# Optimization experiments

Measured on AMD Instinct MI355X. Metric: run time of the kernel, lower is better.

Reference implementation:

```python
import jax, jax.numpy as jnp
import numpy as np

B, C, T = 32, 1024, 1024
BETA = 0.95      # snn.Leaky(beta=0.95)
THR = 1.0        # snntorch Leaky default threshold
SIGMA_INIT = 10.5  # mean of sigma_range (1, 20)


def _gaussian_matrix(sigma, channels):
    # row i is the Gaussian pdf over x=0..C-1 centered at mean=i (vectorized
    # form of the source's per-row Python loop; identical values).
    x = jnp.arange(channels, dtype=jnp.float32)
    u = (x[None, :] - x[:, None]) / sigma  # [C, C]
    coef = 1.0 / (sigma * jnp.sqrt(jnp.asarray(2.0 * jnp.pi, dtype=jnp.float32)))
    return coef * jnp.exp(-0.5 * u * u)


def _spike(u):
    # heaviside(u) forward; ATan surrogate gradient (snntorch default, alpha=2)
    soft = jnp.arctan(jnp.pi * u) / jnp.pi
    hard = (u > 0).astype(u.dtype)
    return soft + jax.lax.stop_gradient(hard - soft)


def setup_inputs() -> dict:
    key = jax.random.key(0)
    inp = jax.random.normal(key, (B, C, T), dtype=jnp.float32)
    sigma = jnp.ones((1,), dtype=jnp.float32) * SIGMA_INIT
    return {"inp": inp, "sigma": sigma}


def reference(inp, sigma):
    # inp: [B, C, T], sigma: [1]
    s = sigma[0]
    w = _gaussian_matrix(s, inp.shape[1])  # computed once: identical at every t
    # I[b,i,t] = x[b,i,t] - sum_j w[i,j] * x[b,j,t]
    I = inp - jnp.einsum('ij,bjt->bit', w, inp)
    I_tbc = jnp.moveaxis(I, 2, 0)  # [T, B, C]

    def step(mem, It):
        # snntorch Leaky (reset_mechanism='subtract'):
        # reset fires on incoming mem, then decay+integrate, then spike.
        reset = _spike(mem - THR)
        mem = BETA * mem + It - reset * THR
        spk = _spike(mem - THR)
        return mem, spk

    mem0 = jnp.zeros(I_tbc.shape[1:], dtype=inp.dtype)  # [B, C]
    _, spks = jax.lax.scan(step, mem0, I_tbc)  # spks: [T, B, C]
    return jnp.moveaxis(spks, 0, 2)  # [B, C, T]
```

## Files before the change

### kernel.cpp

```cpp
#include <hip/hip_runtime.h>
#include <math.h>

#define B_     32
#define C_     1024
#define T_     1024
#define RT     92
#define CT     64
#define TT     64
#define KC     8
#define NTY    8
#define WOFF   (RT + KC - 1)
#define NWT    200
#define NCOLS  (CT + 2*RT)
#define XSTR   252
#define ISTR   65
#define NF4    (NCOLS * (TT/4))

__device__ __forceinline__ float tap_value(float s, int d) {
    float u    = __fdiv_rn((float)d, s);
    float t1   = __fmul_rn(-0.5f, u);
    float t2   = __fmul_rn(t1, u);
    float e    = (float)exp((double)t2);
    float den  = __fmul_rn(s, sqrtf(6.2831854820251465f));
    float coef = __fdiv_rn(1.0f, den);
    return __fmul_rn(coef, e);
}

#define EL(v, i) ((i) == 0 ? (v).x : (i) == 1 ? (v).y : (i) == 2 ? (v).z : (v).w)

#define FMASTEP(A, WA, WB, WC)                                                  \
    do {                                                                        \
        _Pragma("unroll")                                                       \
        for (int qq = 0; qq < 4; ++qq) {                                        \
            float x1 = EL(A, qq);                                               \
            _Pragma("unroll")                                                   \
            for (int k = 0; k < KC; ++k) {                                      \
                const int il = qq + 7 - k;                                      \
                float wv = (il < 4) ? EL(WA, il)                                \
                         : (il < 8) ? EL(WB, il - 4) : EL(WC, il - 8);          \
                acc[k] = fmaf(wv, x1, acc[k]);                                  \
            }                                                                   \
        }                                                                       \
    } while (0)

__global__ __launch_bounds__(512, 4) void snn_v11(
    const float* __restrict__ x, const float* __restrict__ sigma,
    float* __restrict__ out)
{
    __shared__ __align__(16) float xsT[TT * XSTR];
    __shared__ __align__(16) float IsS[NTY * KC * ISTR];

    const int tx   = threadIdx.x;
    const int ty   = threadIdx.y;
    const int flat = ty * 64 + tx;
    const int b    = blockIdx.y;
    const int c0   = blockIdx.x * CT;
    const int rb   = ty * KC;

    const float* xb = x   + (size_t)b * ((size_t)C_ * T_);
    float*       ob = out + (size_t)b * ((size_t)C_ * T_);

    if (flat < NWT) {
        int d = flat - WOFF;
        xsT[(flat >> 2) * XSTR + 248 + (flat & 3)] =
            (d >= -RT && d <= RT) ? tap_value(sigma[0], d) : 0.0f;
    }

    float4 stg[2][4];
    const int rB  = (flat >> 2);
    const int c4B = (flat & 3);

#define STAGE_LOAD(T0)                                                          \
    _Pragma("unroll")                                                           \
    for (int i1 = 0; i1 < 2; ++i1) {                                            \
        _Pragma("unroll")                                                       \
        for (int i2 = 0; i2 < 4; ++i2) {                                        \
            int r  = rB + 128 * i1;                                             \
            int c4 = c4B + 4 * i2;                                              \
            int c  = c0 - RT + r;                                               \
            float4 v = make_float4(0.f, 0.f, 0.f, 0.f);                         \
            if (r < NCOLS && c >= 0 && c < C_)                                  \
                v = *(const float4*)(xb + (size_t)c * T_ + (T0) + c4 * 4);      \
            stg[i1][i2] = v;                                                    \
        }                                                                       \
    }

#define STAGE_WRITE()                                                           \
    _Pragma("unroll")                                                           \
    for (int i1 = 0; i1 < 2; ++i1) {                                            \
        _Pragma("unroll")                                                       \
        for (int i2 = 0; i2 < 4; ++i2) {                                        \
            int r  = rB + 128 * i1;                                             \
            int c4 = c4B + 4 * i2;                                              \
            if (r < NCOLS) {                                                    \
                xsT[(4 * c4 + 0) * XSTR + r] = stg[i1][i2].x;                   \
                xsT[(4 * c4 + 1) * XSTR + r] = stg[i1][i2].y;                   \
                xsT[(4 * c4 + 2) * XSTR + r] = stg[i1][i2].z;                   \
                xsT[(4 * c4 + 3) * XSTR + r] = stg[i1][i2].w;                   \
            }                                                                   \
        }                                                                       \
    }

#define TAPQ(Q) (*(const float4*)(xsT + (Q) * XSTR + 248))

#define PASS(P)                                                                 \
    do {                                                                        \
        float4 w0 = TAPQ(6*(P)+0), w1 = TAPQ(6*(P)+1), w2 = TAPQ(6*(P)+2);      \
        float4 w3 = TAPQ(6*(P)+3), w4 = TAPQ(6*(P)+4), w5 = TAPQ(6*(P)+5);      \
        float4 w6 = TAPQ(6*(P)+6), w7 = TAPQ(6*(P)+7);                          \
        float4 a0 = xq[6*(P)+0], a1 = xq[6*(P)+1], a2 = xq[6*(P)+2];            \
        float4 a3 = xq[6*(P)+3], a4 = xq[6*(P)+4], a5 = xq[6*(P)+5];            \
        FMASTEP(a0, w0, w1, w2);                                                \
        FMASTEP(a1, w1, w2, w3);                                                \
        FMASTEP(a2, w2, w3, w4);                                                \
        FMASTEP(a3, w3, w4, w5);                                                \
        FMASTEP(a4, w4, w5, w6);                                                \
        FMASTEP(a5, w5, w6, w7);                                                \
    } while (0)

    STAGE_LOAD(0);

    float mem = 0.0f;
    float rc  = 0.0f;
    float* strip = IsS + ty * (KC * ISTR);
    const float4* xq = (const float4*)(xsT + tx * XSTR + rb);

#pragma unroll 1
    for (int kk = 0; kk < T_ / TT; ++kk) {
        STAGE_WRITE();
        __syncthreads();

        if (kk < T_ / TT - 1) { STAGE_LOAD((kk + 1) * TT); }

        float acc[KC];
#pragma unroll
        for (int k = 0; k < KC; ++k) acc[k] = 0.0f;

        PASS(0); PASS(1); PASS(2); PASS(3);
        PASS(4); PASS(5); PASS(6); PASS(7);

        {
            float4 xo0 = xq[RT / 4];
            float4 xo1 = xq[RT / 4 + 1];
            strip[0 * ISTR + tx] = __fsub_rn(xo0.x, acc[0]);
            strip[1 * ISTR + tx] = __fsub_rn(xo0.y, acc[1]);
            strip[2 * ISTR + tx] = __fsub_rn(xo0.z, acc[2]);
            strip[3 * ISTR + tx] = __fsub_rn(xo0.w, acc[3]);
            strip[4 * ISTR + tx] = __fsub_rn(xo1.x, acc[4]);
            strip[5 * ISTR + tx] = __fsub_rn(xo1.y, acc[5]);
            strip[6 * ISTR + tx] = __fsub_rn(xo1.z, acc[6]);
            strip[7 * ISTR + tx] = __fsub_rn(xo1.w, acc[7]);
        }
        __syncthreads();

        if (tx < KC) {
            float m = mem, r = rc;
            const float* srow = strip + tx * ISTR;
            float* orow = ob + (size_t)(c0 + rb + tx) * T_ + (size_t)kk * TT;
#pragma unroll 4
            for (int q = 0; q < TT / 4; ++q) {
                float4 s;
#pragma unroll
                for (int qq = 0; qq < 4; ++qq) {
                    float Ivv = srow[4 * q + qq];
                    m = __fsub_rn(__fadd_rn(__fmul_rn(0.95f, m), Ivv), r);
                    float sp = (m > 1.0f) ? 1.0f : 0.0f;
                    r = sp;
                    if (qq == 0) s.x = sp; else if (qq == 1) s.y = sp;
                    else if (qq == 2) s.z = sp; else s.w = sp;
                }
                *(float4*)(orow + 4 * q) = s;
            }
            mem = m; rc = r;
        }
        __syncthreads();
    }
#undef STAGE_LOAD
#undef STAGE_WRITE
#undef TAPQ
#undef PASS
}

extern "C" void kernel_launch(void* const* d_in, const int* in_sizes, int n_in,
                              void* d_out, int out_size, void* d_ws, size_t ws_size,
                              hipStream_t stream) {
    const float* x     = (const float*)d_in[0];
    const float* sigma = (const float*)d_in[1];
    float* out = (float*)d_out;

    dim3 grid(C_ / CT, B_);
    dim3 block(64, NTY);

    snn_v11<<<grid, block, 0, stream>>>(x, sigma, out);
}
```

Before: 183.5 us.

## Use packed f32x2 FMAs with time-pair interleaved shared layout

Restructures the banded Gaussian convolution so each thread handles two adjacent time steps at once, using packed two-wide FMA on vector types (v_pk_fma_f32 on CDNA). Shared memory is re-laid out as time-pair interleaved rows, taps move to a separate small array, and the thread grid changes from 64x8 with 8 channels per thread to 32x16 with 4 channels per thread. The intermediate barrier before the recurrence is removed, since each group now reads only its own strip. This aims to halve FMA instruction count, at the cost of a new layout, possible LDS bank conflicts, and changed register pressure.

```diff
diff --git a/kernel.cpp b/kernel.cpp
--- a/kernel.cpp
+++ b/kernel.cpp
@@ -7,14 +7,18 @@
 #define RT     92
 #define CT     64
 #define TT     64
-#define KC     8
-#define NTY    8
+#define KC     4
+#define NG     16
 #define WOFF   (RT + KC - 1)
-#define NWT    200
+#define NWT    192
 #define NCOLS  (CT + 2*RT)
-#define XSTR   252
-#define ISTR   65
+#define NRP    (TT/2)
+#define XSTR2  500
+#define ISTR   66
 #define NF4    (NCOLS * (TT/4))
+
+typedef float f32x2 __attribute__((ext_vector_type(2)));
+typedef float f32x4 __attribute__((ext_vector_type(4)));
 
 __device__ __forceinline__ float tap_value(float s, int d) {
     float u    = __fdiv_rn((float)d, s);
@@ -27,103 +31,112 @@
 }
 
 #define EL(v, i) ((i) == 0 ? (v).x : (i) == 1 ? (v).y : (i) == 2 ? (v).z : (v).w)
-
-#define FMASTEP(A, WA, WB, WC)                                                  \
+#define SEL4(T0, T1, T2, T3, il)                                                \
+    ((il) < 4 ? EL(T0, (il)) : (il) < 8 ? EL(T1, (il) - 4)                      \
+              : (il) < 12 ? EL(T2, (il) - 8) : EL(T3, (il) - 12))
+
+#if __has_builtin(__builtin_elementwise_fma)
+#define PKFMA(W2, X2, A2) __builtin_elementwise_fma((W2), (X2), (A2))
+#else
+#define PKFMA(W2, X2, A2) (f32x2){fmaf((W2).x,(X2).x,(A2).x), fmaf((W2).y,(X2).y,(A2).y)}
+#endif
+
+#define COLSTEP(XP, ILB, T0, T1, T2, T3)                                        \
     do {                                                                        \
         _Pragma("unroll")                                                       \
-        for (int qq = 0; qq < 4; ++qq) {                                        \
-            float x1 = EL(A, qq);                                               \
-            _Pragma("unroll")                                                   \
-            for (int k = 0; k < KC; ++k) {                                      \
-                const int il = qq + 7 - k;                                      \
-                float wv = (il < 4) ? EL(WA, il)                                \
-                         : (il < 8) ? EL(WB, il - 4) : EL(WC, il - 8);          \
-                acc[k] = fmaf(wv, x1, acc[k]);                                  \
-            }                                                                   \
+        for (int k = 0; k < KC; ++k) {                                          \
+            const int il = (ILB) + 3 - k;                                       \
+            float wv = SEL4(T0, T1, T2, T3, il);                                \
+            f32x2 w2 = {wv, wv};                                                \
+            acc[k] = PKFMA(w2, XP, acc[k]);                                     \
         }                                                                       \
     } while (0)
 
-__global__ __launch_bounds__(512, 4) void snn_v11(
+#define STEP2(XV, LL, T0, T1, T2, T3)                                           \
+    do {                                                                        \
+        f32x2 xlo_ = (XV).xy;                                                   \
+        f32x2 xhi_ = (XV).zw;                                                   \
+        COLSTEP(xlo_, (LL),     T0, T1, T2, T3);                                \
+        COLSTEP(xhi_, (LL) + 1, T0, T1, T2, T3);                                \
+    } while (0)
+
+#define PASS(P)                                                                 \
+    do {                                                                        \
+        f32x4 T0 = wq4[3*(P)+0], T1 = wq4[3*(P)+1];                             \
+        f32x4 T2 = wq4[3*(P)+2], T3 = wq4[3*(P)+3];                             \
+        f32x4 x0 = xr4[6*(P)+0], x1 = xr4[6*(P)+1], x2 = xr4[6*(P)+2];          \
+        f32x4 x3 = xr4[6*(P)+3], x4 = xr4[6*(P)+4], x5 = xr4[6*(P)+5];          \
+        STEP2(x0, 0, T0, T1, T2, T3); STEP2(x1, 2,  T0, T1, T2, T3);            \
+        STEP2(x2, 4, T0, T1, T2, T3); STEP2(x3, 6,  T0, T1, T2, T3);            \
+        STEP2(x4, 8, T0, T1, T2, T3); STEP2(x5, 10, T0, T1, T2, T3);            \
+    } while (0)
+
+#define PASSL()                                                                 \
+    do {                                                                        \
+        f32x4 T0 = wq4[45], T1 = wq4[46], T2 = wq4[47];                         \
+        f32x4 x0 = xr4[90], x1 = xr4[91], x2 = xr4[92], x3 = xr4[93];           \
+        STEP2(x0, 0, T0, T1, T2, T2); STEP2(x1, 2, T0, T1, T2, T2);             \
+        STEP2(x2, 4, T0, T1, T2, T2); STEP2(x3, 6, T0, T1, T2, T2);             \
+    } while (0)
+
+__global__ __launch_bounds__(512, 4) void snn_v12(
     const float* __restrict__ x, const float* __restrict__ sigma,
     float* __restrict__ out)
 {
-    __shared__ __align__(16) float xsT[TT * XSTR];
-    __shared__ __align__(16) float IsS[NTY * KC * ISTR];
-
-    const int tx   = threadIdx.x;
-    const int ty   = threadIdx.y;
-    const int flat = ty * 64 + tx;
+    __shared__ __align__(16) float xsT2[NRP * XSTR2];
+    __shared__ __align__(16) float IsS[NG * KC * ISTR];
+    __shared__ __align__(16) float wtap[NWT];
+
+    const int tp   = threadIdx.x;
+    const int g    = threadIdx.y;
+    const int flat = g * 32 + tp;
     const int b    = blockIdx.y;
     const int c0   = blockIdx.x * CT;
-    const int rb   = ty * KC;
+
+    if (flat < NWT) {
+        int d = flat - WOFF;
+        wtap[flat] = (d >= -RT && d <= RT) ? tap_value(sigma[0], d) : 0.0f;
+    }
 
     const float* xb = x   + (size_t)b * ((size_t)C_ * T_);
     float*       ob = out + (size_t)b * ((size_t)C_ * T_);
 
-    if (flat < NWT) {
-        int d = flat - WOFF;
-        xsT[(flat >> 2) * XSTR + 248 + (flat & 3)] =
-            (d >= -RT && d <= RT) ? tap_value(sigma[0], d) : 0.0f;
-    }
-
-    float4 stg[2][4];
-    const int rB  = (flat >> 2);
-    const int c4B = (flat & 3);
-
-#define STAGE_LOAD(T0)                                                          \
+    f32x4 stg[8];
+
+#define STAGE_LOAD(T0_)                                                         \
     _Pragma("unroll")                                                           \
-    for (int i1 = 0; i1 < 2; ++i1) {                                            \
-        _Pragma("unroll")                                                       \
-        for (int i2 = 0; i2 < 4; ++i2) {                                        \
-            int r  = rB + 128 * i1;                                             \
-            int c4 = c4B + 4 * i2;                                              \
-            int c  = c0 - RT + r;                                               \
-            float4 v = make_float4(0.f, 0.f, 0.f, 0.f);                         \
-            if (r < NCOLS && c >= 0 && c < C_)                                  \
-                v = *(const float4*)(xb + (size_t)c * T_ + (T0) + c4 * 4);      \
-            stg[i1][i2] = v;                                                    \
+    for (int i = 0; i < 8; ++i) {                                               \
+        int e = flat + i * 512;                                                 \
+        f32x4 v = {0.f, 0.f, 0.f, 0.f};                                         \
+        if (e < NF4) {                                                          \
+            int col = e >> 4, tq = e & 15;                                      \
+            int c = c0 - RT + col;                                              \
+            if (c >= 0 && c < C_)                                               \
+                v = *(const f32x4*)(xb + (size_t)c * T_ + (T0_) + tq * 4);      \
         }                                                                       \
+        stg[i] = v;                                                             \
     }
 
 #define STAGE_WRITE()                                                           \
     _Pragma("unroll")                                                           \
-    for (int i1 = 0; i1 < 2; ++i1) {                                            \
-        _Pragma("unroll")                                                       \
-        for (int i2 = 0; i2 < 4; ++i2) {                                        \
-            int r  = rB + 128 * i1;                                             \
-            int c4 = c4B + 4 * i2;                                              \
-            if (r < NCOLS) {                                                    \
-                xsT[(4 * c4 + 0) * XSTR + r] = stg[i1][i2].x;                   \
-                xsT[(4 * c4 + 1) * XSTR + r] = stg[i1][i2].y;                   \
-                xsT[(4 * c4 + 2) * XSTR + r] = stg[i1][i2].z;                   \
-                xsT[(4 * c4 + 3) * XSTR + r] = stg[i1][i2].w;                   \
-            }                                                                   \
+    for (int i = 0; i < 8; ++i) {                                               \
+        int e = flat + i * 512;                                                 \
+        if (e < NF4) {                                                          \
+            int col = e >> 4, tq = e & 15;                                      \
+            f32x2 lo = stg[i].xy;        \
+            f32x2 hi = stg[i].zw;        \
+            *(f32x2*)(xsT2 + (2 * tq + 0) * XSTR2 + 2 * col) = lo;              \
+            *(f32x2*)(xsT2 + (2 * tq + 1) * XSTR2 + 2 * col) = hi;              \
         }                                                                       \
     }
-
-#define TAPQ(Q) (*(const float4*)(xsT + (Q) * XSTR + 248))
-
-#define PASS(P)                                                                 \
-    do {                                                                        \
-        float4 w0 = TAPQ(6*(P)+0), w1 = TAPQ(6*(P)+1), w2 = TAPQ(6*(P)+2);      \
-        float4 w3 = TAPQ(6*(P)+3), w4 = TAPQ(6*(P)+4), w5 = TAPQ(6*(P)+5);      \
-        float4 w6 = TAPQ(6*(P)+6), w7 = TAPQ(6*(P)+7);                          \
-        float4 a0 = xq[6*(P)+0], a1 = xq[6*(P)+1], a2 = xq[6*(P)+2];            \
-        float4 a3 = xq[6*(P)+3], a4 = xq[6*(P)+4], a5 = xq[6*(P)+5];            \
-        FMASTEP(a0, w0, w1, w2);                                                \
-        FMASTEP(a1, w1, w2, w3);                                                \
-        FMASTEP(a2, w2, w3, w4);                                                \
-        FMASTEP(a3, w3, w4, w5);                                                \
-        FMASTEP(a4, w4, w5, w6);                                                \
-        FMASTEP(a5, w5, w6, w7);                                                \
-    } while (0)
 
     STAGE_LOAD(0);
 
     float mem = 0.0f;
     float rc  = 0.0f;
-    float* strip = IsS + ty * (KC * ISTR);
-    const float4* xq = (const float4*)(xsT + tx * XSTR + rb);
+    float* sbase = IsS + g * (KC * ISTR);
+    const f32x4* wq4 = (const f32x4*)wtap;
+    const f32x4* xr4 = (const f32x4*)(xsT2 + (size_t)tp * XSTR2 + 8 * g);
 
 #pragma unroll 1
     for (int kk = 0; kk < T_ / TT; ++kk) {
@@ -132,44 +145,48 @@
 
         if (kk < T_ / TT - 1) { STAGE_LOAD((kk + 1) * TT); }
 
-        float acc[KC];
+        f32x2 acc[KC];
 #pragma unroll
-        for (int k = 0; k < KC; ++k) acc[k] = 0.0f;
-
-        PASS(0); PASS(1); PASS(2); PASS(3);
-        PASS(4); PASS(5); PASS(6); PASS(7);
+        for (int k = 0; k < KC; ++k) acc[k] = (f32x2){0.f, 0.f};
+
+        PASS(0);  PASS(1);  PASS(2);  PASS(3);  PASS(4);
+        PASS(5);  PASS(6);  PASS(7);  PASS(8);  PASS(9);
+        PASS(10); PASS(11); PASS(12); PASS(13); PASS(14);
+        PASSL();
 
         {
-            float4 xo0 = xq[RT / 4];
-            float4 xo1 = xq[RT / 4 + 1];
-            strip[0 * ISTR + tx] = __fsub_rn(xo0.x, acc[0]);
-            strip[1 * ISTR + tx] = __fsub_rn(xo0.y, acc[1]);
-            strip[2 * ISTR + tx] = __fsub_rn(xo0.z, acc[2]);
-            strip[3 * ISTR + tx] = __fsub_rn(xo0.w, acc[3]);
-            strip[4 * ISTR + tx] = __fsub_rn(xo1.x, acc[4]);
-            strip[5 * ISTR + tx] = __fsub_rn(xo1.y, acc[5]);
-            strip[6 * ISTR + tx] = __fsub_rn(xo1.z, acc[6]);
-            strip[7 * ISTR + tx] = __fsub_rn(xo1.w, acc[7]);
+            f32x4 xoA = xr4[46];
+            f32x4 xoB = xr4[47];
+            f32x2 I0 = xoA.xy - acc[0];
+            f32x2 I1 = xoA.zw - acc[1];
+            f32x2 I2 = xoB.xy - acc[2];
+            f32x2 I3 = xoB.zw - acc[3];
+            *(f32x2*)(sbase + 0 * ISTR + 2 * tp) = I0;
+            *(f32x2*)(sbase + 1 * ISTR + 2 * tp) = I1;
+            *(f32x2*)(sbase + 2 * ISTR + 2 * tp) = I2;
+            *(f32x2*)(sbase + 3 * ISTR + 2 * tp) = I3;
         }
-        __syncthreads();
-
-        if (tx < KC) {
+
+        if (tp < KC) {
             float m = mem, r = rc;
-            const float* srow = strip + tx * ISTR;
-            float* orow = ob + (size_t)(c0 + rb + tx) * T_ + (size_t)kk * TT;
+            const float* srow = sbase + tp * ISTR;
+            float* orow = ob + (size_t)(c0 + 4 * g + tp) * T_ + (size_t)kk * TT;
 #pragma unroll 4
             for (int q = 0; q < TT / 4; ++q) {
-                float4 s;
+                f32x2 ia = *(const f32x2*)(srow + 4 * q);
+                f32x2 ib = *(const f32x2*)(srow + 4 * q + 2);
+                f32x4 s;
 #pragma unroll
                 for (int qq = 0; qq < 4; ++qq) {
-                    float Ivv = srow[4 * q + qq];
+                    float Ivv = (qq == 0) ? ia.x : (qq == 1) ? ia.y
+                              : (qq == 2) ? ib.x : ib.y;
                     m = __fsub_rn(__fadd_rn(__fmul_rn(0.95f, m), Ivv), r);
                     float sp = (m > 1.0f) ? 1.0f : 0.0f;
                     r = sp;
                     if (qq == 0) s.x = sp; else if (qq == 1) s.y = sp;
                     else if (qq == 2) s.z = sp; else s.w = sp;
                 }
-                *(float4*)(orow + 4 * q) = s;
+                *(f32x4*)(orow + 4 * q) = s;
             }
             mem = m; rc = r;
         }
@@ -177,8 +194,6 @@
     }
 #undef STAGE_LOAD
 #undef STAGE_WRITE
-#undef TAPQ
-#undef PASS
 }
 
 extern "C" void kernel_launch(void* const* d_in, const int* in_sizes, int n_in,
@@ -189,7 +204,7 @@
     float* out = (float*)d_out;
 
     dim3 grid(C_ / CT, B_);
-    dim3 block(64, NTY);
-
-    snn_v11<<<grid, block, 0, stream>>>(x, sigma, out);
+    dim3 block(32, NG);
+
+    snn_v12<<<grid, block, 0, stream>>>(x, sigma, out);
 }
```

New measurement: 199.5 us. 8.8% more time.

## Rotate tap and input registers to prefetch LDS ahead of FMAs; drop block barrier

Applied to the files above, without the earlier changes.

The banded convolution inner loop becomes 16 three-column passes over rotating register sets. Each pass issues the LDS loads for the next pass's input and tap vectors before doing its own FMAs, which hides LDS latency behind arithmetic and avoids reloading overlapping tap vectors. The __syncthreads between the per-wavefront strip write and the membrane scan is removed, because each strip is written and read by the same 64-thread wavefront. This leans on wave64 lockstep and in-order LDS ordering for correctness, and the live rotating registers raise register pressure under the 512x4 launch bounds.

```diff
diff --git a/kernel.cpp b/kernel.cpp
--- a/kernel.cpp
+++ b/kernel.cpp
@@ -27,23 +27,36 @@
 }
 
 #define EL(v, i) ((i) == 0 ? (v).x : (i) == 1 ? (v).y : (i) == 2 ? (v).z : (v).w)
-
-#define FMASTEP(A, WA, WB, WC)                                                  \
+#define SEL5(il, T0, T1, T2, T3, T4)                                            \
+    ((il) < 4 ? EL(T0, (il)) : (il) < 8 ? EL(T1, (il) - 4)                      \
+     : (il) < 12 ? EL(T2, (il) - 8) : (il) < 16 ? EL(T3, (il) - 12)             \
+     : EL(T4, (il) - 16))
+
+#define COL(XV, CC, T0, T1, T2, T3, T4)                                         \
     do {                                                                        \
+        float x1_ = EL(XV, (CC) & 3);                                           \
         _Pragma("unroll")                                                       \
-        for (int qq = 0; qq < 4; ++qq) {                                        \
-            float x1 = EL(A, qq);                                               \
-            _Pragma("unroll")                                                   \
-            for (int k = 0; k < KC; ++k) {                                      \
-                const int il = qq + 7 - k;                                      \
-                float wv = (il < 4) ? EL(WA, il)                                \
-                         : (il < 8) ? EL(WB, il - 4) : EL(WC, il - 8);          \
-                acc[k] = fmaf(wv, x1, acc[k]);                                  \
-            }                                                                   \
+        for (int k = 0; k < KC; ++k) {                                          \
+            const int il_ = (CC) + 7 - k;                                       \
+            acc[k] = fmaf(SEL5(il_, T0, T1, T2, T3, T4), x1_, acc[k]);          \
         }                                                                       \
     } while (0)
 
-__global__ __launch_bounds__(512, 4) void snn_v11(
+#define PASSX(QB, T0, T1, T2, T3, T4, L0, L1, L2, XA, XB, XC, YA, YB, YC, DOLD) \
+    do {                                                                        \
+        if (DOLD) {                                                             \
+            YA = xq[(QB) + 3]; YB = xq[(QB) + 4]; YC = xq[(QB) + 5];            \
+            L0 = TAPQ((QB) + 5); L1 = TAPQ((QB) + 6); L2 = TAPQ((QB) + 7);      \
+        }                                                                       \
+        COL(XA, 0, T0, T1, T2, T3, T4);  COL(XA, 1, T0, T1, T2, T3, T4);        \
+        COL(XA, 2, T0, T1, T2, T3, T4);  COL(XA, 3, T0, T1, T2, T3, T4);        \
+        COL(XB, 4, T0, T1, T2, T3, T4);  COL(XB, 5, T0, T1, T2, T3, T4);        \
+        COL(XB, 6, T0, T1, T2, T3, T4);  COL(XB, 7, T0, T1, T2, T3, T4);        \
+        COL(XC, 8, T0, T1, T2, T3, T4);  COL(XC, 9, T0, T1, T2, T3, T4);        \
+        COL(XC, 10, T0, T1, T2, T3, T4); COL(XC, 11, T0, T1, T2, T3, T4);       \
+    } while (0)
+
+__global__ __launch_bounds__(512, 4) void snn_v13(
     const float* __restrict__ x, const float* __restrict__ sigma,
     float* __restrict__ out)
 {
@@ -103,21 +116,6 @@
 
 #define TAPQ(Q) (*(const float4*)(xsT + (Q) * XSTR + 248))
 
-#define PASS(P)                                                                 \
-    do {                                                                        \
-        float4 w0 = TAPQ(6*(P)+0), w1 = TAPQ(6*(P)+1), w2 = TAPQ(6*(P)+2);      \
-        float4 w3 = TAPQ(6*(P)+3), w4 = TAPQ(6*(P)+4), w5 = TAPQ(6*(P)+5);      \
-        float4 w6 = TAPQ(6*(P)+6), w7 = TAPQ(6*(P)+7);                          \
-        float4 a0 = xq[6*(P)+0], a1 = xq[6*(P)+1], a2 = xq[6*(P)+2];            \
-        float4 a3 = xq[6*(P)+3], a4 = xq[6*(P)+4], a5 = xq[6*(P)+5];            \
-        FMASTEP(a0, w0, w1, w2);                                                \
-        FMASTEP(a1, w1, w2, w3);                                                \
-        FMASTEP(a2, w2, w3, w4);                                                \
-        FMASTEP(a3, w3, w4, w5);                                                \
-        FMASTEP(a4, w4, w5, w6);                                                \
-        FMASTEP(a5, w5, w6, w7);                                                \
-    } while (0)
-
     STAGE_LOAD(0);
 
     float mem = 0.0f;
@@ -136,8 +134,26 @@
 #pragma unroll
         for (int k = 0; k < KC; ++k) acc[k] = 0.0f;
 
-        PASS(0); PASS(1); PASS(2); PASS(3);
-        PASS(4); PASS(5); PASS(6); PASS(7);
+        float4 n0 = TAPQ(0), n1 = TAPQ(1), n2 = TAPQ(2), n3 = TAPQ(3), n4 = TAPQ(4);
+        float4 x0 = xq[0], x1 = xq[1], x2 = xq[2];
+        float4 n5, n6, n7, x3, x4, x5;
+
+        PASSX(0,  n0,n1,n2,n3,n4, n5,n6,n7, x0,x1,x2, x3,x4,x5, 1);
+        PASSX(3,  n3,n4,n5,n6,n7, n0,n1,n2, x3,x4,x5, x0,x1,x2, 1);
+        PASSX(6,  n6,n7,n0,n1,n2, n3,n4,n5, x0,x1,x2, x3,x4,x5, 1);
+        PASSX(9,  n1,n2,n3,n4,n5, n6,n7,n0, x3,x4,x5, x0,x1,x2, 1);
+        PASSX(12, n4,n5,n6,n7,n0, n1,n2,n3, x0,x1,x2, x3,x4,x5, 1);
+        PASSX(15, n7,n0,n1,n2,n3, n4,n5,n6, x3,x4,x5, x0,x1,x2, 1);
+        PASSX(18, n2,n3,n4,n5,n6, n7,n0,n1, x0,x1,x2, x3,x4,x5, 1);
+        PASSX(21, n5,n6,n7,n0,n1, n2,n3,n4, x3,x4,x5, x0,x1,x2, 1);
+        PASSX(24, n0,n1,n2,n3,n4, n5,n6,n7, x0,x1,x2, x3,x4,x5, 1);
+        PASSX(27, n3,n4,n5,n6,n7, n0,n1,n2, x3,x4,x5, x0,x1,x2, 1);
+        PASSX(30, n6,n7,n0,n1,n2, n3,n4,n5, x0,x1,x2, x3,x4,x5, 1);
+        PASSX(33, n1,n2,n3,n4,n5, n6,n7,n0, x3,x4,x5, x0,x1,x2, 1);
+        PASSX(36, n4,n5,n6,n7,n0, n1,n2,n3, x0,x1,x2, x3,x4,x5, 1);
+        PASSX(39, n7,n0,n1,n2,n3, n4,n5,n6, x3,x4,x5, x0,x1,x2, 1);
+        PASSX(42, n2,n3,n4,n5,n6, n7,n0,n1, x0,x1,x2, x3,x4,x5, 1);
+        PASSX(45, n5,n6,n7,n0,n1, n2,n3,n4, x3,x4,x5, x0,x1,x2, 0);
 
         {
             float4 xo0 = xq[RT / 4];
@@ -151,7 +167,6 @@
             strip[6 * ISTR + tx] = __fsub_rn(xo1.z, acc[6]);
             strip[7 * ISTR + tx] = __fsub_rn(xo1.w, acc[7]);
         }
-        __syncthreads();
 
         if (tx < KC) {
             float m = mem, r = rc;
@@ -178,7 +193,6 @@
 #undef STAGE_LOAD
 #undef STAGE_WRITE
 #undef TAPQ
-#undef PASS
 }
 
 extern "C" void kernel_launch(void* const* d_in, const int* in_sizes, int n_in,
@@ -191,5 +205,5 @@
     dim3 grid(C_ / CT, B_);
     dim3 block(64, NTY);
 
-    snn_v11<<<grid, block, 0, stream>>>(x, sigma, out);
+    snn_v13<<<grid, block, 0, stream>>>(x, sigma, out);
 }
```

Measured after the change: 178.2 us. 1.03x faster.

## Widen per-thread channel register tile to 16 and halve block threads

Applied to the files above, without the earlier changes.

Each thread now computes 16 output channels instead of 8, with 4 wavefronts of 256 threads instead of 8 wavefronts of 512. Each loaded x value and tap quad is reused across twice as many accumulators, which cuts LDS read traffic per FMA. The global staging load is flattened to 16 float4 per thread, and the barrier between the strip write and the scan is dropped, relying on writer and reader being in the same wavefront. The cost is much higher register pressure (16 accumulators plus 16 staged float4), which may lower occupancy. The serial scan also runs on 16 lanes per wave instead of 8.

```diff
diff --git a/kernel.cpp b/kernel.cpp
--- a/kernel.cpp
+++ b/kernel.cpp
@@ -7,10 +7,10 @@
 #define RT     92
 #define CT     64
 #define TT     64
-#define KC     8
-#define NTY    8
+#define KC     16
+#define NTY    4
 #define WOFF   (RT + KC - 1)
-#define NWT    200
+#define NWT    216
 #define NCOLS  (CT + 2*RT)
 #define XSTR   252
 #define ISTR   65
@@ -27,23 +27,49 @@
 }
 
 #define EL(v, i) ((i) == 0 ? (v).x : (i) == 1 ? (v).y : (i) == 2 ? (v).z : (v).w)
-
-#define FMASTEP(A, WA, WB, WC)                                                  \
+#define SEL7(il, W0, W1, W2, W3, W4, W5, W6)                                    \
+    ((il) < 4 ? EL(W0, (il)) : (il) < 8 ? EL(W1, (il) - 4)                      \
+     : (il) < 12 ? EL(W2, (il) - 8) : (il) < 16 ? EL(W3, (il) - 12)             \
+     : (il) < 20 ? EL(W4, (il) - 16) : (il) < 24 ? EL(W5, (il) - 20)            \
+     : EL(W6, (il) - 24))
+
+#define COL16(XV, CC, W0, W1, W2, W3, W4, W5, W6)                               \
     do {                                                                        \
+        float x1_ = EL(XV, (CC) & 3);                                           \
         _Pragma("unroll")                                                       \
-        for (int qq = 0; qq < 4; ++qq) {                                        \
-            float x1 = EL(A, qq);                                               \
-            _Pragma("unroll")                                                   \
-            for (int k = 0; k < KC; ++k) {                                      \
-                const int il = qq + 7 - k;                                      \
-                float wv = (il < 4) ? EL(WA, il)                                \
-                         : (il < 8) ? EL(WB, il - 4) : EL(WC, il - 8);          \
-                acc[k] = fmaf(wv, x1, acc[k]);                                  \
-            }                                                                   \
+        for (int k = 0; k < KC; ++k) {                                          \
+            const int il_ = (CC) + (KC - 1) - k;                                \
+            acc[k] = fmaf(SEL7(il_, W0, W1, W2, W3, W4, W5, W6), x1_, acc[k]);  \
         }                                                                       \
     } while (0)
 
-__global__ __launch_bounds__(512, 4) void snn_v11(
+#define PASS(P)                                                                 \
+    do {                                                                        \
+        float4 w0 = TAPQ(3*(P)+0), w1 = TAPQ(3*(P)+1), w2 = TAPQ(3*(P)+2);      \
+        float4 w3 = TAPQ(3*(P)+3), w4 = TAPQ(3*(P)+4), w5 = TAPQ(3*(P)+5);      \
+        float4 w6 = TAPQ(3*(P)+6);                                              \
+        float4 a0 = xq[3*(P)+0], a1 = xq[3*(P)+1], a2 = xq[3*(P)+2];            \
+        COL16(a0, 0,  w0,w1,w2,w3,w4,w5,w6); COL16(a0, 1,  w0,w1,w2,w3,w4,w5,w6); \
+        COL16(a0, 2,  w0,w1,w2,w3,w4,w5,w6); COL16(a0, 3,  w0,w1,w2,w3,w4,w5,w6); \
+        COL16(a1, 4,  w0,w1,w2,w3,w4,w5,w6); COL16(a1, 5,  w0,w1,w2,w3,w4,w5,w6); \
+        COL16(a1, 6,  w0,w1,w2,w3,w4,w5,w6); COL16(a1, 7,  w0,w1,w2,w3,w4,w5,w6); \
+        COL16(a2, 8,  w0,w1,w2,w3,w4,w5,w6); COL16(a2, 9,  w0,w1,w2,w3,w4,w5,w6); \
+        COL16(a2, 10, w0,w1,w2,w3,w4,w5,w6); COL16(a2, 11, w0,w1,w2,w3,w4,w5,w6); \
+    } while (0)
+
+#define PASSL()                                                                 \
+    do {                                                                        \
+        float4 w0 = TAPQ(48), w1 = TAPQ(49), w2 = TAPQ(50);                     \
+        float4 w3 = TAPQ(51), w4 = TAPQ(52), w5 = TAPQ(53);                     \
+        float4 a0 = xq[48], a1 = xq[49];                                        \
+        COL16(a0, 0, w0,w1,w2,w3,w4,w5,w5); COL16(a0, 1, w0,w1,w2,w3,w4,w5,w5); \
+        COL16(a0, 2, w0,w1,w2,w3,w4,w5,w5); COL16(a0, 3, w0,w1,w2,w3,w4,w5,w5); \
+        COL16(a1, 4, w0,w1,w2,w3,w4,w5,w5); COL16(a1, 5, w0,w1,w2,w3,w4,w5,w5); \
+        COL16(a1, 6, w0,w1,w2,w3,w4,w5,w5); COL16(a1, 7, w0,w1,w2,w3,w4,w5,w5); \
+    } while (0)
+
+__global__ __launch_bounds__(256)
+__attribute__((amdgpu_waves_per_eu(2, 4))) void snn_v15(
     const float* __restrict__ x, const float* __restrict__ sigma,
     float* __restrict__ out)
 {
@@ -66,57 +92,36 @@
             (d >= -RT && d <= RT) ? tap_value(sigma[0], d) : 0.0f;
     }
 
-    float4 stg[2][4];
-    const int rB  = (flat >> 2);
-    const int c4B = (flat & 3);
+    float4 stg[16];
 
 #define STAGE_LOAD(T0)                                                          \
     _Pragma("unroll")                                                           \
-    for (int i1 = 0; i1 < 2; ++i1) {                                            \
-        _Pragma("unroll")                                                       \
-        for (int i2 = 0; i2 < 4; ++i2) {                                        \
-            int r  = rB + 128 * i1;                                             \
-            int c4 = c4B + 4 * i2;                                              \
-            int c  = c0 - RT + r;                                               \
-            float4 v = make_float4(0.f, 0.f, 0.f, 0.f);                         \
-            if (r < NCOLS && c >= 0 && c < C_)                                  \
+    for (int i = 0; i < 16; ++i) {                                              \
+        int e = flat + i * 256;                                                 \
+        float4 v = make_float4(0.f, 0.f, 0.f, 0.f);                             \
+        if (e < NF4) {                                                          \
+            int r = e >> 4, c4 = e & 15;                                        \
+            int c = c0 - RT + r;                                                \
+            if (c >= 0 && c < C_)                                               \
                 v = *(const float4*)(xb + (size_t)c * T_ + (T0) + c4 * 4);      \
-            stg[i1][i2] = v;                                                    \
         }                                                                       \
+        stg[i] = v;                                                             \
     }
 
 #define STAGE_WRITE()                                                           \
     _Pragma("unroll")                                                           \
-    for (int i1 = 0; i1 < 2; ++i1) {                                            \
-        _Pragma("unroll")                                                       \
-        for (int i2 = 0; i2 < 4; ++i2) {                                        \
-            int r  = rB + 128 * i1;                                             \
-            int c4 = c4B + 4 * i2;                                              \
-            if (r < NCOLS) {                                                    \
-                xsT[(4 * c4 + 0) * XSTR + r] = stg[i1][i2].x;                   \
-                xsT[(4 * c4 + 1) * XSTR + r] = stg[i1][i2].y;                   \
-                xsT[(4 * c4 + 2) * XSTR + r] = stg[i1][i2].z;                   \
-                xsT[(4 * c4 + 3) * XSTR + r] = stg[i1][i2].w;                   \
-            }                                                                   \
+    for (int i = 0; i < 16; ++i) {                                              \
+        int e = flat + i * 256;                                                 \
+        if (e < NF4) {                                                          \
+            int r = e >> 4, c4 = e & 15;                                        \
+            xsT[(4 * c4 + 0) * XSTR + r] = stg[i].x;                            \
+            xsT[(4 * c4 + 1) * XSTR + r] = stg[i].y;                            \
+            xsT[(4 * c4 + 2) * XSTR + r] = stg[i].z;                            \
+            xsT[(4 * c4 + 3) * XSTR + r] = stg[i].w;                            \
         }                                                                       \
     }
 
 #define TAPQ(Q) (*(const float4*)(xsT + (Q) * XSTR + 248))
-
-#define PASS(P)                                                                 \
-    do {                                                                        \
-        float4 w0 = TAPQ(6*(P)+0), w1 = TAPQ(6*(P)+1), w2 = TAPQ(6*(P)+2);      \
-        float4 w3 = TAPQ(6*(P)+3), w4 = TAPQ(6*(P)+4), w5 = TAPQ(6*(P)+5);      \
-        float4 w6 = TAPQ(6*(P)+6), w7 = TAPQ(6*(P)+7);                          \
-        float4 a0 = xq[6*(P)+0], a1 = xq[6*(P)+1], a2 = xq[6*(P)+2];            \
-        float4 a3 = xq[6*(P)+3], a4 = xq[6*(P)+4], a5 = xq[6*(P)+5];            \
-        FMASTEP(a0, w0, w1, w2);                                                \
-        FMASTEP(a1, w1, w2, w3);                                                \
-        FMASTEP(a2, w2, w3, w4);                                                \
-        FMASTEP(a3, w3, w4, w5);                                                \
-        FMASTEP(a4, w4, w5, w6);                                                \
-        FMASTEP(a5, w5, w6, w7);                                                \
-    } while (0)
 
     STAGE_LOAD(0);
 
@@ -136,22 +141,31 @@
 #pragma unroll
         for (int k = 0; k < KC; ++k) acc[k] = 0.0f;
 
-        PASS(0); PASS(1); PASS(2); PASS(3);
-        PASS(4); PASS(5); PASS(6); PASS(7);
+        PASS(0);  PASS(1);  PASS(2);  PASS(3);
+        PASS(4);  PASS(5);  PASS(6);  PASS(7);
+        PASS(8);  PASS(9);  PASS(10); PASS(11);
+        PASS(12); PASS(13); PASS(14); PASS(15);
+        PASSL();
 
         {
-            float4 xo0 = xq[RT / 4];
-            float4 xo1 = xq[RT / 4 + 1];
-            strip[0 * ISTR + tx] = __fsub_rn(xo0.x, acc[0]);
-            strip[1 * ISTR + tx] = __fsub_rn(xo0.y, acc[1]);
-            strip[2 * ISTR + tx] = __fsub_rn(xo0.z, acc[2]);
-            strip[3 * ISTR + tx] = __fsub_rn(xo0.w, acc[3]);
-            strip[4 * ISTR + tx] = __fsub_rn(xo1.x, acc[4]);
-            strip[5 * ISTR + tx] = __fsub_rn(xo1.y, acc[5]);
-            strip[6 * ISTR + tx] = __fsub_rn(xo1.z, acc[6]);
-            strip[7 * ISTR + tx] = __fsub_rn(xo1.w, acc[7]);
+            float4 xo0 = xq[23], xo1 = xq[24], xo2 = xq[25], xo3 = xq[26];
+            strip[ 0 * ISTR + tx] = __fsub_rn(xo0.x, acc[0]);
+            strip[ 1 * ISTR + tx] = __fsub_rn(xo0.y, acc[1]);
+            strip[ 2 * ISTR + tx] = __fsub_rn(xo0.z, acc[2]);
+            strip[ 3 * ISTR + tx] = __fsub_rn(xo0.w, acc[3]);
+            strip[ 4 * ISTR + tx] = __fsub_rn(xo1.x, acc[4]);
+            strip[ 5 * ISTR + tx] = __fsub_rn(xo1.y, acc[5]);
+            strip[ 6 * ISTR + tx] = __fsub_rn(xo1.z, acc[6]);
+            strip[ 7 * ISTR + tx] = __fsub_rn(xo1.w, acc[7]);
+            strip[ 8 * ISTR + tx] = __fsub_rn(xo2.x, acc[8]);
+            strip[ 9 * ISTR + tx] = __fsub_rn(xo2.y, acc[9]);
+            strip[10 * ISTR + tx] = __fsub_rn(xo2.z, acc[10]);
+            strip[11 * ISTR + tx] = __fsub_rn(xo2.w, acc[11]);
+            strip[12 * ISTR + tx] = __fsub_rn(xo3.x, acc[12]);
+            strip[13 * ISTR + tx] = __fsub_rn(xo3.y, acc[13]);
+            strip[14 * ISTR + tx] = __fsub_rn(xo3.z, acc[14]);
+            strip[15 * ISTR + tx] = __fsub_rn(xo3.w, acc[15]);
         }
-        __syncthreads();
 
         if (tx < KC) {
             float m = mem, r = rc;
@@ -178,7 +192,6 @@
 #undef STAGE_LOAD
 #undef STAGE_WRITE
 #undef TAPQ
-#undef PASS
 }
 
 extern "C" void kernel_launch(void* const* d_in, const int* in_sizes, int n_in,
@@ -191,5 +204,5 @@
     dim3 grid(C_ / CT, B_);
     dim3 block(64, NTY);
 
-    snn_v11<<<grid, block, 0, stream>>>(x, sigma, out);
+    snn_v15<<<grid, block, 0, stream>>>(x, sigma, out);
 }
```

After: 206.7 us. +12.7%, slower.
